# Performance work log

Measured on AMD Instinct MI355X. Metric: run time of the kernel, lower is better.

Reference implementation:

```python
import jax, jax.numpy as jnp
import numpy as np

H = 128  # hidden size
I = 6    # input size after concat

def setup_inputs() -> dict:
    key = jax.random.key(0)
    ks = jax.random.split(key, 12)
    B, T = 2048, 168
    s_inp = jax.random.normal(ks[0], (B, T, 5), dtype=jnp.float32)
    flow_x = jax.random.normal(ks[1], (B, T, 1), dtype=jnp.float32)
    sc = 1.0 / np.sqrt(H)
    # PyTorch LSTM params: gate order i, f, g, o
    W_ih = jax.random.uniform(ks[2], (4 * H, I), jnp.float32, -sc, sc)
    W_hh = jax.random.uniform(ks[3], (4 * H, H), jnp.float32, -sc, sc)
    b_ih = jax.random.uniform(ks[4], (4 * H,), jnp.float32, -sc, sc)
    b_hh = jax.random.uniform(ks[5], (4 * H,), jnp.float32, -sc, sc)
    sc1 = 1.0 / np.sqrt(128)
    W1 = jax.random.uniform(ks[6], (64, 128), jnp.float32, -sc1, sc1)
    b1 = jax.random.uniform(ks[7], (64,), jnp.float32, -sc1, sc1)
    a1 = jnp.array(0.25, dtype=jnp.float32)  # PReLU weight
    sc2 = 1.0 / np.sqrt(64)
    W2 = jax.random.uniform(ks[8], (1, 64), jnp.float32, -sc2, sc2)
    b2 = jax.random.uniform(ks[9], (1,), jnp.float32, -sc2, sc2)
    a2 = jnp.array(0.25, dtype=jnp.float32)
    return {"s_inp": s_inp, "flow_x": flow_x, "W_ih": W_ih, "W_hh": W_hh,
            "b_ih": b_ih, "b_hh": b_hh, "W1": W1, "b1": b1, "a1": a1,
            "W2": W2, "b2": b2, "a2": a2}

def _prelu(x, a):
    return jnp.where(x >= 0, x, a * x)

def _lstm_last(x, W_ih, W_hh, b_ih, b_hh):
    # x: [B, T, I] -> last hidden state h_T: [B, H]
    B = x.shape[0]
    # precompute input contribution for all timesteps: [T, B, 4H]
    x_gates = jnp.einsum('bti,gi->tbg', x, W_ih) + (b_ih + b_hh)

    def step(carry, xg):
        h, c = carry
        gates = xg + h @ W_hh.T  # [B, 4H]
        i, f, g, o = jnp.split(gates, 4, axis=-1)
        i = jax.nn.sigmoid(i)
        f = jax.nn.sigmoid(f)
        g = jnp.tanh(g)
        o = jax.nn.sigmoid(o)
        c = f * c + i * g
        h = o * jnp.tanh(c)
        return (h, c), None

    h0 = jnp.zeros((B, H), dtype=x.dtype)
    c0 = jnp.zeros((B, H), dtype=x.dtype)
    (h, c), _ = jax.lax.scan(step, (h0, c0), x_gates)
    return h

def reference(s_inp, flow_x, W_ih, W_hh, b_ih, b_hh, W1, b1, a1, W2, b2, a2):
    x = jnp.concatenate([s_inp, flow_x], axis=2)  # [B, T, 6]
    h_last = _lstm_last(x, W_ih, W_hh, b_ih, b_hh)  # [B, 128]
    y = _prelu(h_last @ W1.T + b1, a1)              # [B, 64]
    y = _prelu(y @ W2.T + b2, a2)                   # [B, 1]
    return y
```

## Files before the change

kernel.cpp:

```cpp
#include <hip/hip_runtime.h>


typedef __attribute__((ext_vector_type(8))) short short8;
typedef __attribute__((ext_vector_type(4))) float f32x4;

#define BT 512
#define TS 168
#define HID 128
#define AROW 320
#define NNT 4

__device__ __forceinline__ ushort bf_hi(float v) {
    return (ushort)(__float_as_uint(v) >> 16);
}
__device__ __forceinline__ ushort bf_lo(float v) {
    unsigned h = __float_as_uint(v) & 0xFFFF0000u;
    float l = v - __uint_as_float(h);
    return (ushort)(__float_as_uint(l) >> 16);
}
__device__ __forceinline__ float sigm_f(float x) {
    return __fdividef(1.f, 1.f + __expf(-x));
}
__device__ __forceinline__ float tanh_f(float x) {
    return 1.f - __fdividef(2.f, __expf(2.f * x) + 1.f);
}

__global__ __launch_bounds__(BT, 2) void lstm_mfma7_kernel(
    const float* __restrict__ s_inp,
    const float* __restrict__ flow_x,
    const float* __restrict__ W_ih,
    const float* __restrict__ W_hh,
    const float* __restrict__ b_ih,
    const float* __restrict__ b_hh,
    const float* __restrict__ W1,
    const float* __restrict__ b1,
    const float* __restrict__ a1p,
    const float* __restrict__ W2,
    const float* __restrict__ b2,
    const float* __restrict__ a2p,
    float* __restrict__ out)
{
    __shared__ float xs[8][TS][6];
    __shared__ __align__(16) ushort hA[8 * AROW];
    __shared__ float y1s[8][64];

    const int t = threadIdx.x;
    const int w = t >> 6;
    const int l = t & 63;
    const int l15 = l & 15;
    const int l4 = l >> 4;
    const int row_base = blockIdx.x * 8;

    short8 P1s[5][NNT], P2s[5][NNT];
    #pragma unroll
    for (int nt = 0; nt < NNT; ++nt) {
        const int gc = nt * HID + w * 16 + l15;
        const float bias = b_ih[gc] + b_hh[gc];
        #pragma unroll
        for (int q = 0; q < 4; ++q) {
            #pragma unroll
            for (int j = 0; j < 8; ++j) {
                float v = W_hh[gc * HID + q * 32 + l4 * 8 + j];
                P1s[q][nt][j] = (short)bf_hi(v);
                P2s[q][nt][j] = (short)bf_lo(v);
            }
        }
        #pragma unroll
        for (int j = 0; j < 8; ++j) {
            int u = l4 * 8 + j;
            float v = (u < 6)  ? W_ih[gc * 6 + u]
                    : (u < 12) ? W_ih[gc * 6 + (u - 6)]
                    : (u == 12) ? bias : 0.f;
            P1s[4][nt][j] = (short)bf_hi(v);
            P2s[4][nt][j] = (short)bf_lo(v);
        }
    }

    for (int idx = t; idx < 8 * TS * 5; idx += BT) {
        int r = idx / (TS * 5), rem = idx % (TS * 5);
        xs[r][rem / 5][rem % 5] = s_inp[(size_t)row_base * (TS * 5) + idx];
    }
    for (int idx = t; idx < 8 * TS; idx += BT) {
        xs[idx / TS][idx % TS][5] = flow_x[(size_t)row_base * TS + idx];
    }
    for (int idx = t; idx < 8 * AROW / 2; idx += BT)
        ((unsigned*)hA)[idx] = 0u;
    __syncthreads();

    if (t < 8) {
        int byte = (2 * 268) ^ ((t & 7) << 4);
        hA[t * AROW + (byte >> 1)] = 0x3F80;
    }
    const bool xhi = (t < 48);
    const bool xlo = (t >= 64 && t < 112);
    const int xu = xhi ? t : (t - 64);
    const int xr = (xu < 48) ? (xu / 6) : 0;
    const int xi = (xu < 48) ? (xu % 6) : 0;
    const int xslot = xhi ? (256 + xi) : (262 + xi);
    const int xw_idx = xr * AROW + ((((2 * xslot) ^ ((xr & 7) << 4))) >> 1);
    if (xhi | xlo) {
        float v = xs[xr][0][xi];
        hA[xw_idx] = xhi ? bf_hi(v) : bf_lo(v);
    }

    const int arow = l15 & 7;
    const int a_base = arow * AROW;
    const int a_swz = arow << 4;
    const int ch = w * 16 + l15;
    const bool lowhalf = (l < 32);
    const int rbase = (l4 & 1) * 4 + (lowhalf ? 0 : 2);
    const int row0 = rbase, row1 = rbase + 1;
    const int hw0 = row0 * AROW + ((((2 * ch) ^ (row0 << 4))) >> 1);
    const int hw1 = row1 * AROW + ((((2 * ch) ^ (row1 << 4))) >> 1);

    float c0 = 0.f, c1 = 0.f, h0f = 0.f, h1f = 0.f;

    for (int s = 0; s < TS; ++s) {
        __syncthreads();

        f32x4 acc1[NNT], acc2[NNT];
        #pragma unroll
        for (int nt = 0; nt < NNT; ++nt) {
            acc1[nt] = (f32x4){0.f, 0.f, 0.f, 0.f};
            acc2[nt] = (f32x4){0.f, 0.f, 0.f, 0.f};
        }

        #pragma unroll
        for (int kk = 0; kk < 9; ++kk) {
            const int q = (kk < 4) ? kk : ((kk < 8) ? kk - 4 : 4);
            int off = ((kk * 64 + l4 * 16) ^ a_swz) >> 1;
            short8 a = *(const short8*)(hA + a_base + off);
            #pragma unroll
            for (int nt = 0; nt < NNT; ++nt)
                acc1[nt] = __builtin_amdgcn_mfma_f32_16x16x32_bf16(a, P1s[q][nt], acc1[nt], 0, 0, 0);
            if (kk < 4 || kk == 8) {
                #pragma unroll
                for (int nt = 0; nt < NNT; ++nt)
                    acc2[nt] = __builtin_amdgcn_mfma_f32_16x16x32_bf16(a, P2s[q][nt], acc2[nt], 0, 0, 0);
            }
        }

        f32x4 am[NNT];
        #pragma unroll
        for (int nt = 0; nt < NNT; ++nt) {
            #pragma unroll
            for (int e = 0; e < 4; ++e) am[nt][e] = acc1[nt][e] + acc2[nt][e];
        }

        float gi0 = lowhalf ? am[0][0] : am[0][2];
        float gf0 = lowhalf ? am[1][0] : am[1][2];
        float gg0 = lowhalf ? am[2][0] : am[2][2];
        float go0 = lowhalf ? am[3][0] : am[3][2];
        float gi1 = lowhalf ? am[0][1] : am[0][3];
        float gf1 = lowhalf ? am[1][1] : am[1][3];
        float gg1 = lowhalf ? am[2][1] : am[2][3];
        float go1 = lowhalf ? am[3][1] : am[3][3];

        {
            float ia = sigm_f(gi0);
            float fa = sigm_f(gf0);
            float ga = tanh_f(gg0);
            float oa = sigm_f(go0);
            c0 = fa * c0 + ia * ga;
            h0f = oa * tanh_f(c0);
        }
        {
            float ia = sigm_f(gi1);
            float fa = sigm_f(gf1);
            float ga = tanh_f(gg1);
            float oa = sigm_f(go1);
            c1 = fa * c1 + ia * ga;
            h1f = oa * tanh_f(c1);
        }

        hA[hw0] = bf_hi(h0f);
        hA[hw0 + 128] = bf_lo(h0f);
        hA[hw1] = bf_hi(h1f);
        hA[hw1 + 128] = bf_lo(h1f);

        if ((xhi | xlo) && s + 1 < TS) {
            float v = xs[xr][s + 1][xi];
            hA[xw_idx] = xhi ? bf_hi(v) : bf_lo(v);
        }
    }
    __syncthreads();

    float* hfin = (float*)xs;
    hfin[row0 * HID + ch] = h0f;
    hfin[row1 * HID + ch] = h1f;
    __syncthreads();

    {
        int r = t >> 6, j = t & 63;
        const float4* wrow = (const float4*)(W1 + j * HID);
        const float4* hr = (const float4*)(hfin + r * HID);
        float acc = b1[j];
        #pragma unroll
        for (int q = 0; q < HID / 4; ++q) {
            float4 a = hr[q], b = wrow[q];
            acc += a.x * b.x + a.y * b.y + a.z * b.z + a.w * b.w;
        }
        float av = a1p[0];
        y1s[r][j] = (acc >= 0.f) ? acc : av * acc;
    }
    __syncthreads();

    if (t < 8) {
        const float4* w2 = (const float4*)W2;
        const float4* yr = (const float4*)&y1s[t][0];
        float acc = 0.f;
        #pragma unroll
        for (int q = 0; q < 64 / 4; ++q) {
            float4 a = yr[q], b = w2[q];
            acc += a.x * b.x + a.y * b.y + a.z * b.z + a.w * b.w;
        }
        acc += b2[0];
        float av = a2p[0];
        out[row_base + t] = (acc >= 0.f) ? acc : av * acc;
    }
}

extern "C" void kernel_launch(void* const* d_in, const int* in_sizes, int n_in,
                              void* d_out, int out_size, void* d_ws, size_t ws_size,
                              hipStream_t stream) {
    const float* s_inp  = (const float*)d_in[0];
    const float* flow_x = (const float*)d_in[1];
    const float* W_ih   = (const float*)d_in[2];
    const float* W_hh   = (const float*)d_in[3];
    const float* b_ih   = (const float*)d_in[4];
    const float* b_hh   = (const float*)d_in[5];
    const float* W1     = (const float*)d_in[6];
    const float* b1     = (const float*)d_in[7];
    const float* a1     = (const float*)d_in[8];
    const float* W2     = (const float*)d_in[9];
    const float* b2     = (const float*)d_in[10];
    const float* a2     = (const float*)d_in[11];
    float* out = (float*)d_out;

    dim3 grid(2048 / 8);
    dim3 block(BT);
    lstm_mfma7_kernel<<<grid, block, 0, stream>>>(
        s_inp, flow_x, W_ih, W_hh, b_ih, b_hh, W1, b1, a1, W2, b2, a2, out);
}
```

Before: 264.3 us.

## Split batch rows into two ping-pong groups to overlap MFMA with gate math

The 8 batch rows per block are split into two groups of 4, each with its own hA buffer. In each step the MFMA chain for one group is interleaved with the activation and cell-state update of the other, so the matrix and vector units can overlap instead of running back to back. The separate hi/lo accumulators are merged into one accumulator per group. This adds a second barrier per timestep, and each MFMA now uses only 4 of its 16 A rows, so half the MFMA rows are wasted compared with the previous 8-row packing.

New measurement: 366.0 us. +38.5%, slower.

```diff
diff --git a/kernel.cpp b/kernel.cpp
--- a/kernel.cpp
+++ b/kernel.cpp
@@ -8,6 +8,7 @@
 #define TS 168
 #define HID 128
 #define AROW 320
+#define GBUF (4 * AROW)
 #define NNT 4
 
 __device__ __forceinline__ ushort bf_hi(float v) {
@@ -24,8 +25,15 @@
 __device__ __forceinline__ float tanh_f(float x) {
     return 1.f - __fdividef(2.f, __expf(2.f * x) + 1.f);
 }
-
-__global__ __launch_bounds__(BT, 2) void lstm_mfma7_kernel(
+__device__ __forceinline__ float sel4(f32x4 v, int q) {
+    float r = v[0];
+    r = (q == 1) ? v[1] : r;
+    r = (q == 2) ? v[2] : r;
+    r = (q == 3) ? v[3] : r;
+    return r;
+}
+
+__global__ __launch_bounds__(BT, 2) void lstm_mfma9_kernel(
     const float* __restrict__ s_inp,
     const float* __restrict__ flow_x,
     const float* __restrict__ W_ih,
@@ -41,7 +49,7 @@
     float* __restrict__ out)
 {
     __shared__ float xs[8][TS][6];
-    __shared__ __align__(16) ushort hA[8 * AROW];
+    __shared__ __align__(16) ushort hA[2 * GBUF];
     __shared__ float y1s[8][64];
 
     const int t = threadIdx.x;
@@ -83,48 +91,55 @@
     for (int idx = t; idx < 8 * TS; idx += BT) {
         xs[idx / TS][idx % TS][5] = flow_x[(size_t)row_base * TS + idx];
     }
-    for (int idx = t; idx < 8 * AROW / 2; idx += BT)
+    for (int idx = t; idx < 2 * GBUF / 2; idx += BT)
         ((unsigned*)hA)[idx] = 0u;
     __syncthreads();
 
     if (t < 8) {
-        int byte = (2 * 268) ^ ((t & 7) << 4);
-        hA[t * AROW + (byte >> 1)] = 0x3F80;
-    }
-    const bool xhi = (t < 48);
-    const bool xlo = (t >= 64 && t < 112);
-    const int xu = xhi ? t : (t - 64);
-    const int xr = (xu < 48) ? (xu / 6) : 0;
-    const int xi = (xu < 48) ? (xu % 6) : 0;
-    const int xslot = xhi ? (256 + xi) : (262 + xi);
-    const int xw_idx = xr * AROW + ((((2 * xslot) ^ ((xr & 7) << 4))) >> 1);
-    if (xhi | xlo) {
-        float v = xs[xr][0][xi];
-        hA[xw_idx] = xhi ? bf_hi(v) : bf_lo(v);
-    }
-
-    const int arow = l15 & 7;
+        int b = t >> 2, r = t & 3;
+        int byte = (2 * 268) ^ (r << 4);
+        hA[b * GBUF + r * AROW + (byte >> 1)] = 0x3F80;
+    }
+    {
+        const bool ih = (t < 48);
+        const bool il = (t >= 64 && t < 112);
+        if (ih | il) {
+            int xu = ih ? t : (t - 64);
+            int xr = xu / 6, xi = xu % 6;
+            int b = xr >> 2, lr = xr & 3;
+            int slot = ih ? (256 + xi) : (262 + xi);
+            int idx = b * GBUF + lr * AROW + ((((2 * slot) ^ (lr << 4))) >> 1);
+            float v = xs[xr][0][xi];
+            hA[idx] = ih ? bf_hi(v) : bf_lo(v);
+        }
+    }
+
+    const int arow = l15 & 3;
     const int a_base = arow * AROW;
     const int a_swz = arow << 4;
     const int ch = w * 16 + l15;
-    const bool lowhalf = (l < 32);
-    const int rbase = (l4 & 1) * 4 + (lowhalf ? 0 : 2);
-    const int row0 = rbase, row1 = rbase + 1;
-    const int hw0 = row0 * AROW + ((((2 * ch) ^ (row0 << 4))) >> 1);
-    const int hw1 = row1 * AROW + ((((2 * ch) ^ (row1 << 4))) >> 1);
-
-    float c0 = 0.f, c1 = 0.f, h0f = 0.f, h1f = 0.f;
+    const int hw = l4 * AROW + ((((2 * ch) ^ (l4 << 4))) >> 1);
+    const bool sxh = (t < 24);
+    const bool sxl = (t >= 64 && t < 88);
+    const int sxu = sxh ? t : (t - 64);
+    const int sxr = (sxu < 24) ? (sxu / 6) : 0;
+    const int sxi = (sxu < 24) ? (sxu % 6) : 0;
+    const int sxslot = sxh ? (256 + sxi) : (262 + sxi);
+    const int sxw = sxr * AROW + ((((2 * sxslot) ^ (sxr << 4))) >> 1);
+
+    float cG0 = 0.f, cG1 = 0.f, hG0 = 0.f, hG1 = 0.f;
+    f32x4 accA[NNT], accB[NNT];
+    #pragma unroll
+    for (int nt = 0; nt < NNT; ++nt) {
+        accA[nt] = (f32x4){0.f, 0.f, 0.f, 0.f};
+        accB[nt] = (f32x4){0.f, 0.f, 0.f, 0.f};
+    }
 
     for (int s = 0; s < TS; ++s) {
         __syncthreads();
 
-        f32x4 acc1[NNT], acc2[NNT];
-        #pragma unroll
-        for (int nt = 0; nt < NNT; ++nt) {
-            acc1[nt] = (f32x4){0.f, 0.f, 0.f, 0.f};
-            acc2[nt] = (f32x4){0.f, 0.f, 0.f, 0.f};
-        }
-
+        #pragma unroll
+        for (int nt = 0; nt < NNT; ++nt) accA[nt] = (f32x4){0.f, 0.f, 0.f, 0.f};
         #pragma unroll
         for (int kk = 0; kk < 9; ++kk) {
             const int q = (kk < 4) ? kk : ((kk < 8) ? kk - 4 : 4);
@@ -132,62 +147,71 @@
             short8 a = *(const short8*)(hA + a_base + off);
             #pragma unroll
             for (int nt = 0; nt < NNT; ++nt)
-                acc1[nt] = __builtin_amdgcn_mfma_f32_16x16x32_bf16(a, P1s[q][nt], acc1[nt], 0, 0, 0);
+                accA[nt] = __builtin_amdgcn_mfma_f32_16x16x32_bf16(a, P1s[q][nt], accA[nt], 0, 0, 0);
             if (kk < 4 || kk == 8) {
                 #pragma unroll
                 for (int nt = 0; nt < NNT; ++nt)
-                    acc2[nt] = __builtin_amdgcn_mfma_f32_16x16x32_bf16(a, P2s[q][nt], acc2[nt], 0, 0, 0);
+                    accA[nt] = __builtin_amdgcn_mfma_f32_16x16x32_bf16(a, P2s[q][nt], accA[nt], 0, 0, 0);
             }
         }
-
-        f32x4 am[NNT];
-        #pragma unroll
-        for (int nt = 0; nt < NNT; ++nt) {
+        if (s > 0) {
+            float gi = sel4(accB[0], l4), gf = sel4(accB[1], l4);
+            float gg = sel4(accB[2], l4), go = sel4(accB[3], l4);
+            float ia = sigm_f(gi), fa = sigm_f(gf), ga = tanh_f(gg), oa = sigm_f(go);
+            cG1 = fa * cG1 + ia * ga;
+            hG1 = oa * tanh_f(cG1);
+            hA[GBUF + hw] = bf_hi(hG1);
+            hA[GBUF + hw + 128] = bf_lo(hG1);
+        }
+        if (sxh | sxl) {
+            float v = xs[4 + sxr][s][sxi];
+            hA[GBUF + sxw] = sxh ? bf_hi(v) : bf_lo(v);
+        }
+
+        __syncthreads();
+
+        #pragma unroll
+        for (int nt = 0; nt < NNT; ++nt) accB[nt] = (f32x4){0.f, 0.f, 0.f, 0.f};
+        #pragma unroll
+        for (int kk = 0; kk < 9; ++kk) {
+            const int q = (kk < 4) ? kk : ((kk < 8) ? kk - 4 : 4);
+            int off = ((kk * 64 + l4 * 16) ^ a_swz) >> 1;
+            short8 a = *(const short8*)(hA + GBUF + a_base + off);
             #pragma unroll
-            for (int e = 0; e < 4; ++e) am[nt][e] = acc1[nt][e] + acc2[nt][e];
-        }
-
-        float gi0 = lowhalf ? am[0][0] : am[0][2];
-        float gf0 = lowhalf ? am[1][0] : am[1][2];
-        float gg0 = lowhalf ? am[2][0] : am[2][2];
-        float go0 = lowhalf ? am[3][0] : am[3][2];
-        float gi1 = lowhalf ? am[0][1] : am[0][3];
-        float gf1 = lowhalf ? am[1][1] : am[1][3];
-        float gg1 = lowhalf ? am[2][1] : am[2][3];
-        float go1 = lowhalf ? am[3][1] : am[3][3];
-
+            for (int nt = 0; nt < NNT; ++nt)
+                accB[nt] = __builtin_amdgcn_mfma_f32_16x16x32_bf16(a, P1s[q][nt], accB[nt], 0, 0, 0);
+            if (kk < 4 || kk == 8) {
+                #pragma unroll
+                for (int nt = 0; nt < NNT; ++nt)
+                    accB[nt] = __builtin_amdgcn_mfma_f32_16x16x32_bf16(a, P2s[q][nt], accB[nt], 0, 0, 0);
+            }
+        }
         {
-            float ia = sigm_f(gi0);
-            float fa = sigm_f(gf0);
-            float ga = tanh_f(gg0);
-            float oa = sigm_f(go0);
-            c0 = fa * c0 + ia * ga;
-            h0f = oa * tanh_f(c0);
-        }
-        {
-            float ia = sigm_f(gi1);
-            float fa = sigm_f(gf1);
-            float ga = tanh_f(gg1);
-            float oa = sigm_f(go1);
-            c1 = fa * c1 + ia * ga;
-            h1f = oa * tanh_f(c1);
-        }
-
-        hA[hw0] = bf_hi(h0f);
-        hA[hw0 + 128] = bf_lo(h0f);
-        hA[hw1] = bf_hi(h1f);
-        hA[hw1 + 128] = bf_lo(h1f);
-
-        if ((xhi | xlo) && s + 1 < TS) {
-            float v = xs[xr][s + 1][xi];
-            hA[xw_idx] = xhi ? bf_hi(v) : bf_lo(v);
-        }
-    }
-    __syncthreads();
+            float gi = sel4(accA[0], l4), gf = sel4(accA[1], l4);
+            float gg = sel4(accA[2], l4), go = sel4(accA[3], l4);
+            float ia = sigm_f(gi), fa = sigm_f(gf), ga = tanh_f(gg), oa = sigm_f(go);
+            cG0 = fa * cG0 + ia * ga;
+            hG0 = oa * tanh_f(cG0);
+            hA[hw] = bf_hi(hG0);
+            hA[hw + 128] = bf_lo(hG0);
+        }
+        if ((sxh | sxl) && s + 1 < TS) {
+            float v = xs[sxr][s + 1][sxi];
+            hA[sxw] = sxh ? bf_hi(v) : bf_lo(v);
+        }
+    }
+
+    {
+        float gi = sel4(accB[0], l4), gf = sel4(accB[1], l4);
+        float gg = sel4(accB[2], l4), go = sel4(accB[3], l4);
+        float ia = sigm_f(gi), fa = sigm_f(gf), ga = tanh_f(gg), oa = sigm_f(go);
+        cG1 = fa * cG1 + ia * ga;
+        hG1 = oa * tanh_f(cG1);
+    }
 
     float* hfin = (float*)xs;
-    hfin[row0 * HID + ch] = h0f;
-    hfin[row1 * HID + ch] = h1f;
+    hfin[l4 * HID + ch] = hG0;
+    hfin[(4 + l4) * HID + ch] = hG1;
     __syncthreads();
 
     {
@@ -239,6 +263,6 @@
 
     dim3 grid(2048 / 8);
     dim3 block(BT);
-    lstm_mfma7_kernel<<<grid, block, 0, stream>>>(
+    lstm_mfma9_kernel<<<grid, block, 0, stream>>>(
         s_inp, flow_x, W_ih, W_hh, b_ih, b_hh, W1, b1, a1, W2, b2, a2, out);
 }
```
